# Optimization experiments

Measured on AMD Instinct MI355X. Metric: run time of the kernel, lower is better.

Reference implementation:

```python
import jax, jax.numpy as jnp
import numpy as np

D_MODEL = 1024
NUM_HEADS = 16


def setup_inputs() -> dict:
    key = jax.random.key(0)
    ks = jax.random.split(key, 11)
    B, L, D = 1, 4096, D_MODEL
    s = 1.0 / np.sqrt(D)
    inp = {
        "Q": jax.random.normal(ks[0], (B, L, D), jnp.float32),
        "K": jax.random.normal(ks[1], (B, L, D), jnp.float32),
        "V": jax.random.normal(ks[2], (B, L, D), jnp.float32),
        "w_q": jax.random.normal(ks[3], (D, D), jnp.float32) * s,
        "b_q": jax.random.normal(ks[4], (D,), jnp.float32) * s,
        "w_k": jax.random.normal(ks[5], (D, D), jnp.float32) * s,
        "b_k": jax.random.normal(ks[6], (D,), jnp.float32) * s,
        "w_v": jax.random.normal(ks[7], (D, D), jnp.float32) * s,
        "b_v": jax.random.normal(ks[8], (D,), jnp.float32) * s,
        "w_o": jax.random.normal(ks[9], (D, D), jnp.float32) * s,
        "b_o": jax.random.normal(ks[10], (D,), jnp.float32) * s,
    }
    return inp


def _split_heads(x, n_heads):
    B, L, D = x.shape
    return x.reshape(B, L, n_heads, D // n_heads).transpose(0, 2, 1, 3)  # (B,H,L,Dh)


def reference(Q, K, V, w_q, b_q, w_k, b_k, w_v, b_v, w_o, b_o):
    H = NUM_HEADS
    # QKV projections (torch Linear: x @ W.T + b)
    q = _split_heads(Q @ w_q.T + b_q, H)
    k = _split_heads(K @ w_k.T + b_k, H)
    v = _split_heads(V @ w_v.T + b_v, H)
    d_h = q.shape[-1]
    scores = jnp.einsum("bhqd,bhkd->bhqk", q, k) / jnp.sqrt(jnp.float32(d_h))
    attn = jax.nn.softmax(scores, axis=-1)
    out = jnp.einsum("bhqk,bhkd->bhqd", attn, v)  # (B,H,L,Dh)
    B, _, L, _ = out.shape
    out = out.transpose(0, 2, 1, 3).reshape(B, L, H * d_h)
    return out @ w_o.T + b_o
```

## Files before the change

### kernel.cpp

```cpp
#include <hip/hip_runtime.h>
#include <hip/hip_bf16.h>
#include <stdint.h>

#define D_MODEL 1024
#define NHEAD   16
#define DH      64

typedef __attribute__((ext_vector_type(8))) short bf16x8;
typedef __attribute__((ext_vector_type(4))) float f32x4;

__device__ __forceinline__ ushort f2bf(float f) {
    __hip_bfloat16 h = __float2bfloat16(f);
    return *reinterpret_cast<ushort*>(&h);
}

__device__ __forceinline__ void gload_lds16(const void* g, void* l) {
    __builtin_amdgcn_global_load_lds(
        (const __attribute__((address_space(1))) void*)g,
        (__attribute__((address_space(3))) void*)l, 16, 0, 0);
}

__device__ __forceinline__ bf16x8 load8f(const float* p) {
    const float4 a = *(const float4*)p;
    const float4 b = *(const float4*)(p + 4);
    bf16x8 r;
    r[0] = (short)f2bf(a.x); r[1] = (short)f2bf(a.y);
    r[2] = (short)f2bf(a.z); r[3] = (short)f2bf(a.w);
    r[4] = (short)f2bf(b.x); r[5] = (short)f2bf(b.y);
    r[6] = (short)f2bf(b.z); r[7] = (short)f2bf(b.w);
    return r;
}

__global__ __launch_bounds__(256) void cvt_w_kernel(
    const float* __restrict__ w0, const float* __restrict__ w1,
    const float* __restrict__ w2, const float* __restrict__ w3,
    ushort* __restrict__ out)
{
    const int g = blockIdx.x * 256 + threadIdx.x;
    const int m = g >> 17;
    const int off = (g & 131071) * 8;
    const float* src = (m == 0) ? w0 : (m == 1) ? w1 : (m == 2) ? w2 : w3;
    *(bf16x8*)(out + (size_t)m * 1048576 + off) = load8f(src + off);
}

__global__ __launch_bounds__(256) void cvt_all_kernel(
    const float* __restrict__ w0, const float* __restrict__ w1,
    const float* __restrict__ w2, const float* __restrict__ w3,
    const float* __restrict__ X0, const float* __restrict__ X1,
    const float* __restrict__ X2,
    ushort* __restrict__ Wb,
    ushort* __restrict__ Qb, ushort* __restrict__ Kb, ushort* __restrict__ Vb,
    int igrp)
{
    const int g = blockIdx.x * 256 + threadIdx.x;
    if (g < 524288) {
        const int m = g >> 17;
        const int off = (g & 131071) * 8;
        const float* src = (m == 0) ? w0 : (m == 1) ? w1 : (m == 2) ? w2 : w3;
        *(bf16x8*)(Wb + (size_t)m * 1048576 + off) = load8f(src + off);
    } else {
        const int g2 = g - 524288;
        if (g2 >= 3 * igrp) return;
        const int m = g2 / igrp;
        const int off = (g2 - m * igrp) * 8;
        const float* src = (m == 0) ? X0 : (m == 1) ? X1 : X2;
        ushort* dst = (m == 0) ? Qb : (m == 1) ? Kb : Vb;
        *(bf16x8*)(dst + off) = load8f(src + off);
    }
}

__device__ __forceinline__ void storeC(float*  C, size_t i, float v) { C[i] = v; }
__device__ __forceinline__ void storeC(ushort* C, size_t i, float v) { C[i] = (short)f2bf(v); }

__device__ __forceinline__ void xcd_swizzle(int& bx, int& by) {
    if (gridDim.x == 8 && (gridDim.y & 7) == 0) {
        const int fid   = by * 8 + bx;
        const int xcd   = fid & 7;
        const int local = fid >> 3;
        const int rpx   = gridDim.y >> 3;
        by = xcd * rpx + (local >> 3);
        bx = local & 7;
    }
}

template<int NW, bool A_F32, typename TX, typename TOUT>
__device__ __forceinline__ void gemm_core(
    const TX* __restrict__ X,
    const ushort* __restrict__ Wb,
    const float* __restrict__ Bias,
    TOUT* __restrict__ C,
    int M, int N, int K, float scale,
    short* As, short* Bs)
{
    const int tid  = threadIdx.x;
    const int w    = tid >> 6;
    const int lane = tid & 63;
    const int quad = lane >> 4;
    const int l15  = lane & 15;
    const int wr   = (NW == 4) ? (w >> 1) : (w >> 2);
    const int wc   = (NW == 4) ? (w & 1)  : (w & 3);
    const int NJ   = (NW == 4) ? 4 : 2;
    const int colw = (NW == 4) ? 64 : 32;

    int bx = blockIdx.x, by = blockIdx.y;
    xcd_swizzle(bx, by);
    const int m0 = by * 128;
    const int n0 = bx * 128;

    f32x4 acc[4][4] = {};

    for (int k0 = 0; k0 < K; k0 += 32) {
        __syncthreads();
        #pragma unroll
        for (int c = 0; c < 8 / NW; ++c) {
            int chunk = w * (8 / NW) + c;
            int row   = chunk * 16 + (lane >> 2);
            gload_lds16(Wb + (size_t)(n0 + row) * K + k0 + (lane & 3) * 8,
                        &Bs[chunk * 512]);
        }
        if constexpr (A_F32) {
            #pragma unroll
            for (int c = 0; c < 2; ++c) {
                int idx = c * 256 + tid;
                int row = idx >> 2;
                int col = (idx & 3) * 8;
                *(bf16x8*)&As[row * 32 + col] =
                    load8f((const float*)X + (size_t)(m0 + row) * K + k0 + col);
            }
        } else {
            #pragma unroll
            for (int c = 0; c < 8 / NW; ++c) {
                int chunk = w * (8 / NW) + c;
                int row   = chunk * 16 + (lane >> 2);
                gload_lds16((const ushort*)X + (size_t)(m0 + row) * K + k0 + (lane & 3) * 8,
                            &As[chunk * 512]);
            }
        }
        __syncthreads();

        bf16x8 af[4], bfr[4];
        #pragma unroll
        for (int i = 0; i < 4; ++i)
            af[i] = *(const bf16x8*)&As[(wr * 64 + i * 16 + l15) * 32 + quad * 8];
        #pragma unroll
        for (int j = 0; j < NJ; ++j)
            bfr[j] = *(const bf16x8*)&Bs[(wc * colw + j * 16 + l15) * 32 + quad * 8];
        #pragma unroll
        for (int i = 0; i < 4; ++i)
            #pragma unroll
            for (int j = 0; j < NJ; ++j)
                acc[i][j] = __builtin_amdgcn_mfma_f32_16x16x32_bf16(af[i], bfr[j], acc[i][j], 0, 0, 0);
    }

    float bias[4];
    #pragma unroll
    for (int j = 0; j < NJ; ++j)
        bias[j] = Bias[n0 + wc * colw + j * 16 + l15];

    #pragma unroll
    for (int i = 0; i < 4; ++i) {
        int row = m0 + wr * 64 + i * 16 + quad * 4;
        #pragma unroll
        for (int j = 0; j < NJ; ++j) {
            int col = n0 + wc * colw + j * 16 + l15;
            #pragma unroll
            for (int r = 0; r < 4; ++r)
                storeC(C, (size_t)(row + r) * N + col, (acc[i][j][r] + bias[j]) * scale);
        }
    }
}

__global__ __launch_bounds__(256) void qkv_proj_f32_kernel(
    const float* __restrict__ Qin, const float* __restrict__ Kin,
    const float* __restrict__ Vin,
    const ushort* __restrict__ Wb,
    const float* __restrict__ Bq, const float* __restrict__ Bk,
    const float* __restrict__ Bv,
    ushort* qo, ushort* ko, ushort* vo, int L)
{
    __shared__ short As[4096];
    __shared__ short Bs[4096];
    const int z = blockIdx.z;
    const float *X, *B; ushort* C;
    float scale = 1.0f;
    if (z == 0)      { X = Qin; B = Bq; C = qo; scale = 0.125f * 1.44269504088896f; }
    else if (z == 1) { X = Kin; B = Bk; C = ko; }
    else             { X = Vin; B = Bv; C = vo; }
    gemm_core<4, true, float, ushort>(X, Wb + (size_t)z * 1048576, B, C,
                                      L, D_MODEL, D_MODEL, scale, As, Bs);
}

__global__ __launch_bounds__(256) void qkv_proj_bf16_kernel(
    const ushort* __restrict__ Qb, const ushort* __restrict__ Kb,
    const ushort* __restrict__ Vb,
    const ushort* __restrict__ Wb,
    const float* __restrict__ Bq, const float* __restrict__ Bk,
    const float* __restrict__ Bv,
    ushort* qo, ushort* ko, ushort* vo, int L)
{
    __shared__ short As[4096];
    __shared__ short Bs[4096];
    const int z = blockIdx.z;
    const ushort *X; const float* B; ushort* C;
    float scale = 1.0f;
    if (z == 0)      { X = Qb; B = Bq; C = qo; scale = 0.125f * 1.44269504088896f; }
    else if (z == 1) { X = Kb; B = Bk; C = ko; }
    else             { X = Vb; B = Bv; C = vo; }
    gemm_core<4, false, ushort, ushort>(X, Wb + (size_t)z * 1048576, B, C,
                                        L, D_MODEL, D_MODEL, scale, As, Bs);
}

__global__ __launch_bounds__(512) void out_proj_kernel(
    const ushort* __restrict__ Xa, const ushort* __restrict__ Wb,
    const float* __restrict__ Bo, float* out, int L)
{
    __shared__ short As[4096];
    __shared__ short Bs[4096];
    gemm_core<8, false, ushort, float>(Xa, Wb + (size_t)3 * 1048576, Bo, out,
                                       L, D_MODEL, D_MODEL, 1.0f, As, Bs);
}

__global__ __launch_bounds__(512) void attn_kernel(
    const ushort* __restrict__ Qw,
    const ushort* __restrict__ Kw,
    const ushort* __restrict__ Vw,
    ushort* __restrict__ Ow, int L)
{
    __shared__ short Ks[64 * 64];
    __shared__ short Vs[64 * 64];
    __shared__ short Ps[8][16 * 64];

    const int tid  = threadIdx.x;
    const int w    = tid >> 6;
    const int lane = tid & 63;
    const int quad = lane >> 4;
    const int l15  = lane & 15;
    const int h    = blockIdx.y;
    const int q0   = blockIdx.x * 128;

    const ushort* qp = Qw + (size_t)(q0 + w * 16 + l15) * D_MODEL + h * DH + quad * 8;
    bf16x8 qf0 = *(const bf16x8*)(qp);
    bf16x8 qf1 = *(const bf16x8*)(qp + 32);

    const int kkey = tid >> 3;
    const int kc8  = tid & 7;
    const int vkey = lane;
    const int vdh  = w * 8;

    const int krswz0 = ((quad    ) ^ (l15 & 7)) * 8;
    const int krswz1 = ((quad + 4) ^ (l15 & 7)) * 8;

    f32x4 o[4] = {};
    float m_run = -3e38f, l_run = 0.f;
    const float thr = 8.0f;

    const ushort* kptr = Kw + (size_t)kkey * D_MODEL + h * DH + kc8 * 8;
    const ushort* vptr = Vw + (size_t)vkey * D_MODEL + h * DH + vdh;
    bf16x8 kreg = *(const bf16x8*)kptr;
    bf16x8 vreg = *(const bf16x8*)vptr;

    for (int key0 = 0; key0 < L; key0 += 64) {
        __syncthreads();
        *(bf16x8*)&Ks[kkey * 64 + ((kc8 ^ (kkey & 7)) * 8)] = kreg;
        #pragma unroll
        for (int i = 0; i < 8; ++i)
            Vs[(vdh + i) * 64 + (((vkey >> 3) ^ i) * 8) + (vkey & 7)] = vreg[i];
        __syncthreads();

        if (key0 + 64 < L) {
            kptr += (size_t)64 * D_MODEL;
            vptr += (size_t)64 * D_MODEL;
            kreg = *(const bf16x8*)kptr;
            vreg = *(const bf16x8*)vptr;
        }

        f32x4 st[4];
        __builtin_amdgcn_s_setprio(1);
        #pragma unroll
        for (int kt = 0; kt < 4; ++kt) {
            const int kr = (kt * 16 + l15) * 64;
            bf16x8 kf0 = *(const bf16x8*)&Ks[kr + krswz0];
            bf16x8 kf1 = *(const bf16x8*)&Ks[kr + krswz1];
            f32x4 z = {};
            z = __builtin_amdgcn_mfma_f32_16x16x32_bf16(kf0, qf0, z, 0, 0, 0);
            z = __builtin_amdgcn_mfma_f32_16x16x32_bf16(kf1, qf1, z, 0, 0, 0);
            st[kt] = z;
        }
        __builtin_amdgcn_s_setprio(0);

        float mx = st[0][0];
        #pragma unroll
        for (int kt = 0; kt < 4; ++kt)
            #pragma unroll
            for (int r = 0; r < 4; ++r)
                mx = fmaxf(mx, st[kt][r]);
        mx = fmaxf(mx, __shfl_xor(mx, 16));
        mx = fmaxf(mx, __shfl_xor(mx, 32));

        if (!__all(mx <= m_run + thr)) {
            const float mnew  = fmaxf(m_run, mx);
            const float alpha = __builtin_amdgcn_exp2f(m_run - mnew);
            m_run = mnew;
            l_run *= alpha;
            float a[4];
            #pragma unroll
            for (int r = 0; r < 4; ++r)
                a[r] = __shfl(alpha, (lane & 48) | (quad * 4 + r));
            #pragma unroll
            for (int dt = 0; dt < 4; ++dt)
                #pragma unroll
                for (int r = 0; r < 4; ++r)
                    o[dt][r] *= a[r];
        }

        float rs = 0.f;
        #pragma unroll
        for (int kt = 0; kt < 4; ++kt) {
            float p0 = __builtin_amdgcn_exp2f(st[kt][0] - m_run);
            float p1 = __builtin_amdgcn_exp2f(st[kt][1] - m_run);
            float p2 = __builtin_amdgcn_exp2f(st[kt][2] - m_run);
            float p3 = __builtin_amdgcn_exp2f(st[kt][3] - m_run);
            rs += (p0 + p1) + (p2 + p3);
            uint2 pk;
            pk.x = (uint32_t)f2bf(p0) | ((uint32_t)f2bf(p1) << 16);
            pk.y = (uint32_t)f2bf(p2) | ((uint32_t)f2bf(p3) << 16);
            const int G = kt * 2 + (quad >> 1);
            *(uint2*)&Ps[w][l15 * 64 + ((G ^ (l15 & 7)) * 8) + (quad & 1) * 4] = pk;
        }
        l_run += rs;

        __builtin_amdgcn_s_setprio(1);
        #pragma unroll
        for (int f = 0; f < 2; ++f) {
            bf16x8 pf = *(const bf16x8*)&Ps[w][l15 * 64 + (((f * 4 + quad) ^ (l15 & 7)) * 8)];
            #pragma unroll
            for (int dt = 0; dt < 4; ++dt) {
                bf16x8 vf = *(const bf16x8*)&Vs[(dt * 16 + l15) * 64 + (((f * 4 + quad) ^ (l15 & 7)) * 8)];
                o[dt] = __builtin_amdgcn_mfma_f32_16x16x32_bf16(pf, vf, o[dt], 0, 0, 0);
            }
        }
        __builtin_amdgcn_s_setprio(0);
    }

    l_run += __shfl_xor(l_run, 16);
    l_run += __shfl_xor(l_run, 32);
    const float inv = 1.f / l_run;
    #pragma unroll
    for (int r = 0; r < 4; ++r) {
        const float linv = __shfl(inv, (lane & 48) | (quad * 4 + r));
        const int row = q0 + w * 16 + quad * 4 + r;
        #pragma unroll
        for (int dt = 0; dt < 4; ++dt) {
            int col = h * DH + dt * 16 + l15;
            Ow[(size_t)row * D_MODEL + col] = (short)f2bf(o[dt][r] * linv);
        }
    }
}

extern "C" void kernel_launch(void* const* d_in, const int* in_sizes, int n_in,
                              void* d_out, int out_size, void* d_ws, size_t ws_size,
                              hipStream_t stream) {
    const float* Q   = (const float*)d_in[0];
    const float* K   = (const float*)d_in[1];
    const float* V   = (const float*)d_in[2];
    const float* w_q = (const float*)d_in[3];
    const float* b_q = (const float*)d_in[4];
    const float* w_k = (const float*)d_in[5];
    const float* b_k = (const float*)d_in[6];
    const float* w_v = (const float*)d_in[7];
    const float* b_v = (const float*)d_in[8];
    const float* w_o = (const float*)d_in[9];
    const float* b_o = (const float*)d_in[10];
    float* out = (float*)d_out;

    const int L = in_sizes[0] / D_MODEL;
    const size_t mat = (size_t)L * D_MODEL;

    ushort* Wb   = (ushort*)d_ws;
    ushort* q_ws = (ushort*)d_out;
    ushort* k_ws = q_ws + mat;
    const bool ext = ws_size >= (size_t)40 * 1024 * 1024;

    ushort *a_ws, *v_ws, *Qb = nullptr, *Kb = nullptr, *Vb = nullptr;
    if (ext) {
        Vb   = (ushort*)d_ws + 4 * 1048576;
        v_ws = Vb + mat;
        Qb   = v_ws + mat;
        Kb   = Qb + mat;
        a_ws = Vb;
    } else {
        a_ws = (ushort*)d_ws + 4 * 1048576;
        v_ws = a_ws + mat;
    }

    dim3 gqkv(D_MODEL / 128, L / 128, 3);
    if (ext) {
        const int igrp = (int)(mat / 8);
        const int total = 524288 + 3 * igrp;
        cvt_all_kernel<<<dim3((total + 255) / 256), dim3(256), 0, stream>>>(
            w_q, w_k, w_v, w_o, Q, K, V, Wb, Qb, Kb, Vb, igrp);
        qkv_proj_bf16_kernel<<<gqkv, dim3(256), 0, stream>>>(Qb, Kb, Vb, Wb,
                                                             b_q, b_k, b_v,
                                                             q_ws, k_ws, v_ws, L);
    } else {
        cvt_w_kernel<<<dim3(2048), dim3(256), 0, stream>>>(w_q, w_k, w_v, w_o, Wb);
        qkv_proj_f32_kernel<<<gqkv, dim3(256), 0, stream>>>(Q, K, V, Wb,
                                                            b_q, b_k, b_v,
                                                            q_ws, k_ws, v_ws, L);
    }
    dim3 gattn(L / 128, NHEAD);
    attn_kernel<<<gattn, dim3(512), 0, stream>>>(q_ws, k_ws, v_ws, a_ws, L);
    dim3 gout(D_MODEL / 128, L / 128);
    out_proj_kernel<<<gout, dim3(512), 0, stream>>>(a_ws, Wb, b_o, out, L);
}
```

Measured before the change: 277.5 us.

## Use 32x32x16 MFMA in attention and keep P in registers via permlane32 swap

```diff
diff --git a/kernel.cpp b/kernel.cpp
--- a/kernel.cpp
+++ b/kernel.cpp
@@ -8,6 +8,7 @@
 
 typedef __attribute__((ext_vector_type(8))) short bf16x8;
 typedef __attribute__((ext_vector_type(4))) float f32x4;
+typedef __attribute__((ext_vector_type(16))) float f32x16;
 
 __device__ __forceinline__ ushort f2bf(float f) {
     __hip_bfloat16 h = __float2bfloat16(f);
@@ -220,7 +221,7 @@
                                        L, D_MODEL, D_MODEL, 1.0f, As, Bs);
 }
 
-__global__ __launch_bounds__(512) void attn_kernel(
+__global__ __launch_bounds__(256) void attn_kernel(
     const ushort* __restrict__ Qw,
     const ushort* __restrict__ Kw,
     const ushort* __restrict__ Vw,
@@ -228,73 +229,79 @@
 {
     __shared__ short Ks[64 * 64];
     __shared__ short Vs[64 * 64];
-    __shared__ short Ps[8][16 * 64];
 
     const int tid  = threadIdx.x;
     const int w    = tid >> 6;
     const int lane = tid & 63;
-    const int quad = lane >> 4;
-    const int l15  = lane & 15;
+    const int l31  = lane & 31;
+    const int hi   = lane >> 5;
     const int h    = blockIdx.y;
     const int q0   = blockIdx.x * 128;
 
-    const ushort* qp = Qw + (size_t)(q0 + w * 16 + l15) * D_MODEL + h * DH + quad * 8;
-    bf16x8 qf0 = *(const bf16x8*)(qp);
-    bf16x8 qf1 = *(const bf16x8*)(qp + 32);
-
-    const int kkey = tid >> 3;
-    const int kc8  = tid & 7;
-    const int vkey = lane;
-    const int vdh  = w * 8;
-
-    const int krswz0 = ((quad    ) ^ (l15 & 7)) * 8;
-    const int krswz1 = ((quad + 4) ^ (l15 & 7)) * 8;
-
-    f32x4 o[4] = {};
+    const int qrow = q0 + w * 32 + l31;
+    bf16x8 qf[4];
+    #pragma unroll
+    for (int s = 0; s < 4; ++s)
+        qf[s] = *(const bf16x8*)(Qw + (size_t)qrow * D_MODEL + h * DH + s * 16 + hi * 8);
+
+    const int kkey = tid >> 2;
+    const int kc   = tid & 3;
+    const int vkey = tid & 63;
+    const int w4   = tid >> 6;
+
+    const int kw0 = kkey * 64 + ((kc ^ (kkey & 7)) * 8);
+    const int kw1 = kkey * 64 + (((kc + 4) ^ (kkey & 7)) * 8);
+
+    f32x16 o0 = {}, o1 = {};
     float m_run = -3e38f, l_run = 0.f;
     const float thr = 8.0f;
 
-    const ushort* kptr = Kw + (size_t)kkey * D_MODEL + h * DH + kc8 * 8;
-    const ushort* vptr = Vw + (size_t)vkey * D_MODEL + h * DH + vdh;
-    bf16x8 kreg = *(const bf16x8*)kptr;
-    bf16x8 vreg = *(const bf16x8*)vptr;
+    const ushort* kp = Kw + (size_t)kkey * D_MODEL + h * DH + kc * 8;
+    const ushort* vp = Vw + (size_t)vkey * D_MODEL + h * DH + w4 * 8;
+    bf16x8 kr0 = *(const bf16x8*)kp;
+    bf16x8 kr1 = *(const bf16x8*)(kp + 32);
+    bf16x8 vr0 = *(const bf16x8*)vp;
+    bf16x8 vr1 = *(const bf16x8*)(vp + 32);
+
+    const int swz7 = l31 & 7;
 
     for (int key0 = 0; key0 < L; key0 += 64) {
         __syncthreads();
-        *(bf16x8*)&Ks[kkey * 64 + ((kc8 ^ (kkey & 7)) * 8)] = kreg;
-        #pragma unroll
-        for (int i = 0; i < 8; ++i)
-            Vs[(vdh + i) * 64 + (((vkey >> 3) ^ i) * 8) + (vkey & 7)] = vreg[i];
+        *(bf16x8*)&Ks[kw0] = kr0;
+        *(bf16x8*)&Ks[kw1] = kr1;
+        #pragma unroll
+        for (int i = 0; i < 8; ++i) {
+            const int sw = (((vkey >> 3) ^ i) * 8) + (vkey & 7);
+            Vs[(w4 * 8 + i) * 64 + sw]      = vr0[i];
+            Vs[(w4 * 8 + 32 + i) * 64 + sw] = vr1[i];
+        }
         __syncthreads();
 
         if (key0 + 64 < L) {
-            kptr += (size_t)64 * D_MODEL;
-            vptr += (size_t)64 * D_MODEL;
-            kreg = *(const bf16x8*)kptr;
-            vreg = *(const bf16x8*)vptr;
-        }
-
-        f32x4 st[4];
+            kp += (size_t)64 * D_MODEL;
+            vp += (size_t)64 * D_MODEL;
+            kr0 = *(const bf16x8*)kp;  kr1 = *(const bf16x8*)(kp + 32);
+            vr0 = *(const bf16x8*)vp;  vr1 = *(const bf16x8*)(vp + 32);
+        }
+
+        f32x16 st0 = {}, st1 = {};
         __builtin_amdgcn_s_setprio(1);
         #pragma unroll
-        for (int kt = 0; kt < 4; ++kt) {
-            const int kr = (kt * 16 + l15) * 64;
-            bf16x8 kf0 = *(const bf16x8*)&Ks[kr + krswz0];
-            bf16x8 kf1 = *(const bf16x8*)&Ks[kr + krswz1];
-            f32x4 z = {};
-            z = __builtin_amdgcn_mfma_f32_16x16x32_bf16(kf0, qf0, z, 0, 0, 0);
-            z = __builtin_amdgcn_mfma_f32_16x16x32_bf16(kf1, qf1, z, 0, 0, 0);
-            st[kt] = z;
+        for (int s = 0; s < 4; ++s) {
+            const int ch = ((s * 2 + hi) ^ swz7) * 8;
+            bf16x8 kf0 = *(const bf16x8*)&Ks[l31 * 64 + ch];
+            bf16x8 kf1 = *(const bf16x8*)&Ks[(32 + l31) * 64 + ch];
+            st0 = __builtin_amdgcn_mfma_f32_32x32x16_bf16(kf0, qf[s], st0, 0, 0, 0);
+            st1 = __builtin_amdgcn_mfma_f32_32x32x16_bf16(kf1, qf[s], st1, 0, 0, 0);
         }
         __builtin_amdgcn_s_setprio(0);
 
-        float mx = st[0][0];
-        #pragma unroll
-        for (int kt = 0; kt < 4; ++kt)
-            #pragma unroll
-            for (int r = 0; r < 4; ++r)
-                mx = fmaxf(mx, st[kt][r]);
-        mx = fmaxf(mx, __shfl_xor(mx, 16));
+        float mx = st0[0];
+        #pragma unroll
+        for (int r = 0; r < 16; ++r) {
+            mx = fmaxf(mx, st0[r]);
+            mx = fmaxf(mx, st1[r]);
+        }
         mx = fmaxf(mx, __shfl_xor(mx, 32));
 
         if (!__all(mx <= m_run + thr)) {
@@ -302,58 +309,62 @@
             const float alpha = __builtin_amdgcn_exp2f(m_run - mnew);
             m_run = mnew;
             l_run *= alpha;
-            float a[4];
-            #pragma unroll
-            for (int r = 0; r < 4; ++r)
-                a[r] = __shfl(alpha, (lane & 48) | (quad * 4 + r));
-            #pragma unroll
-            for (int dt = 0; dt < 4; ++dt)
-                #pragma unroll
-                for (int r = 0; r < 4; ++r)
-                    o[dt][r] *= a[r];
-        }
-
-        float rs = 0.f;
-        #pragma unroll
-        for (int kt = 0; kt < 4; ++kt) {
-            float p0 = __builtin_amdgcn_exp2f(st[kt][0] - m_run);
-            float p1 = __builtin_amdgcn_exp2f(st[kt][1] - m_run);
-            float p2 = __builtin_amdgcn_exp2f(st[kt][2] - m_run);
-            float p3 = __builtin_amdgcn_exp2f(st[kt][3] - m_run);
-            rs += (p0 + p1) + (p2 + p3);
-            uint2 pk;
-            pk.x = (uint32_t)f2bf(p0) | ((uint32_t)f2bf(p1) << 16);
-            pk.y = (uint32_t)f2bf(p2) | ((uint32_t)f2bf(p3) << 16);
-            const int G = kt * 2 + (quad >> 1);
-            *(uint2*)&Ps[w][l15 * 64 + ((G ^ (l15 & 7)) * 8) + (quad & 1) * 4] = pk;
-        }
-        l_run += rs;
+            #pragma unroll
+            for (int r = 0; r < 16; ++r) {
+                const int qr = (r & 3) + 8 * (r >> 2) + 4 * hi;
+                const float a = __shfl(alpha, qr);
+                o0[r] *= a;
+                o1[r] *= a;
+            }
+        }
+
+        bf16x8 pa[4];
+        float ls = 0.f;
+        auto pack = [&](const f32x16& stk, bf16x8* dst) {
+            float p[16];
+            #pragma unroll
+            for (int r = 0; r < 16; ++r) {
+                p[r] = __builtin_amdgcn_exp2f(stk[r] - m_run);
+                ls += p[r];
+            }
+            uint32_t u[8];
+            #pragma unroll
+            for (int i = 0; i < 8; ++i)
+                u[i] = (uint32_t)f2bf(p[2 * i]) | ((uint32_t)f2bf(p[2 * i + 1]) << 16);
+            asm volatile("v_permlane32_swap_b32 %0, %1" : "+v"(u[0]), "+v"(u[2]));
+            asm volatile("v_permlane32_swap_b32 %0, %1" : "+v"(u[1]), "+v"(u[3]));
+            asm volatile("v_permlane32_swap_b32 %0, %1" : "+v"(u[4]), "+v"(u[6]));
+            asm volatile("v_permlane32_swap_b32 %0, %1" : "+v"(u[5]), "+v"(u[7]));
+            uint32_t* d0 = (uint32_t*)&dst[0];
+            d0[0] = u[0]; d0[1] = u[1]; d0[2] = u[2]; d0[3] = u[3];
+            uint32_t* d1 = (uint32_t*)&dst[1];
+            d1[0] = u[4]; d1[1] = u[5]; d1[2] = u[6]; d1[3] = u[7];
+        };
+        pack(st0, &pa[0]);
+        pack(st1, &pa[2]);
+        l_run += ls;
 
         __builtin_amdgcn_s_setprio(1);
         #pragma unroll
-        for (int f = 0; f < 2; ++f) {
-            bf16x8 pf = *(const bf16x8*)&Ps[w][l15 * 64 + (((f * 4 + quad) ^ (l15 & 7)) * 8)];
-            #pragma unroll
-            for (int dt = 0; dt < 4; ++dt) {
-                bf16x8 vf = *(const bf16x8*)&Vs[(dt * 16 + l15) * 64 + (((f * 4 + quad) ^ (l15 & 7)) * 8)];
-                o[dt] = __builtin_amdgcn_mfma_f32_16x16x32_bf16(pf, vf, o[dt], 0, 0, 0);
-            }
+        for (int ks = 0; ks < 4; ++ks) {
+            const int kb = ((ks * 2 + hi) ^ swz7) * 8;
+            bf16x8 vf0 = *(const bf16x8*)&Vs[l31 * 64 + kb];
+            bf16x8 vf1 = *(const bf16x8*)&Vs[(32 + l31) * 64 + kb];
+            o0 = __builtin_amdgcn_mfma_f32_32x32x16_bf16(pa[ks], vf0, o0, 0, 0, 0);
+            o1 = __builtin_amdgcn_mfma_f32_32x32x16_bf16(pa[ks], vf1, o1, 0, 0, 0);
         }
         __builtin_amdgcn_s_setprio(0);
     }
 
-    l_run += __shfl_xor(l_run, 16);
     l_run += __shfl_xor(l_run, 32);
     const float inv = 1.f / l_run;
     #pragma unroll
-    for (int r = 0; r < 4; ++r) {
-        const float linv = __shfl(inv, (lane & 48) | (quad * 4 + r));
-        const int row = q0 + w * 16 + quad * 4 + r;
-        #pragma unroll
-        for (int dt = 0; dt < 4; ++dt) {
-            int col = h * DH + dt * 16 + l15;
-            Ow[(size_t)row * D_MODEL + col] = (short)f2bf(o[dt][r] * linv);
-        }
+    for (int r = 0; r < 16; ++r) {
+        const int qr   = (r & 3) + 8 * (r >> 2) + 4 * hi;
+        const float li = __shfl(inv, qr);
+        const size_t row = (size_t)(q0 + w * 32 + qr) * D_MODEL + h * DH;
+        Ow[row + l31]      = (short)f2bf(o0[r] * li);
+        Ow[row + 32 + l31] = (short)f2bf(o1[r] * li);
     }
 }
 
@@ -393,23 +404,24 @@
         v_ws = a_ws + mat;
     }
 
-    dim3 gqkv(D_MODEL / 128, L / 128, 3);
     if (ext) {
         const int igrp = (int)(mat / 8);
         const int total = 524288 + 3 * igrp;
         cvt_all_kernel<<<dim3((total + 255) / 256), dim3(256), 0, stream>>>(
             w_q, w_k, w_v, w_o, Q, K, V, Wb, Qb, Kb, Vb, igrp);
+        dim3 gqkv(D_MODEL / 128, L / 128, 3);
         qkv_proj_bf16_kernel<<<gqkv, dim3(256), 0, stream>>>(Qb, Kb, Vb, Wb,
                                                              b_q, b_k, b_v,
                                                              q_ws, k_ws, v_ws, L);
     } else {
         cvt_w_kernel<<<dim3(2048), dim3(256), 0, stream>>>(w_q, w_k, w_v, w_o, Wb);
+        dim3 gqkv(D_MODEL / 128, L / 128, 3);
         qkv_proj_f32_kernel<<<gqkv, dim3(256), 0, stream>>>(Q, K, V, Wb,
                                                             b_q, b_k, b_v,
                                                             q_ws, k_ws, v_ws, L);
     }
     dim3 gattn(L / 128, NHEAD);
-    attn_kernel<<<gattn, dim3(512), 0, stream>>>(q_ws, k_ws, v_ws, a_ws, L);
+    attn_kernel<<<gattn, dim3(256), 0, stream>>>(q_ws, k_ws, v_ws, a_ws, L);
     dim3 gout(D_MODEL / 128, L / 128);
     out_proj_kernel<<<gout, dim3(512), 0, stream>>>(a_ws, Wb, b_o, out, L);
 }
```

New measurement: 287.5 us. 3.6% more time.
